# Performance work log

Hardware: AMD Instinct MI355X
Metric: run time of the kernel (lower is better)

## Reference

```python
import jax, jax.numpy as jnp
import numpy as np

N_NODES = 20000
N_EDGES = 320000
N_GRAPHS = 64
IN_FEAT = 64
HIDDEN = 256
GRID = 4
NUM_LAYERS = 4  # -> 3 Fourier message-passing layers
NEG_SLOPE = 0.01  # nn.LeakyReLU default


def setup_inputs() -> dict:
    key = jax.random.key(0)
    ks = jax.random.split(key, 8)
    h = jax.random.normal(ks[0], (N_NODES, IN_FEAT), dtype=jnp.float32)
    src = jax.random.randint(ks[1], (N_EDGES,), 0, N_NODES, dtype=jnp.int32)
    dst = jax.random.randint(ks[2], (N_EDGES,), 0, N_NODES, dtype=jnp.int32)
    graph_ids = jnp.sort(jax.random.randint(ks[3], (N_NODES,), 0, N_GRAPHS, dtype=jnp.int32))
    # KAN_polynomial(in_feat, hidden, degree=grid_feat), init randn/(sqrt(in)*sqrt(deg))
    W_line = jax.random.normal(ks[4], (HIDDEN, IN_FEAT, GRID + 1), dtype=jnp.float32) / (
        np.sqrt(IN_FEAT) * np.sqrt(GRID))
    # 3 NaiveFourierKANLayer coeffs [2, out, in, grid]
    fourier_coeffs = jax.random.normal(ks[5], (NUM_LAYERS - 1, 2, HIDDEN, HIDDEN, GRID),
                                       dtype=jnp.float32) / (np.sqrt(HIDDEN) * np.sqrt(GRID))
    # Readout KAN_polynomial(hidden, 1, degree=1, addbias=True)
    W_out = jax.random.normal(ks[6], (1, HIDDEN, 2), dtype=jnp.float32) / np.sqrt(HIDDEN)
    b_out = jnp.zeros((1, 1), dtype=jnp.float32)
    return {"h": h, "src": src, "dst": dst, "graph_ids": graph_ids,
            "W_line": W_line, "fourier_coeffs": fourier_coeffs,
            "W_out": W_out, "b_out": b_out}


def kan_polynomial(x, coeffs, bias=None):
    # x: [b, in], coeffs: [out, in, deg+1]
    deg = coeffs.shape[-1] - 1
    powers = jnp.stack([x ** i for i in range(deg + 1)], axis=-1)  # [b, in, deg+1]
    y = jnp.einsum('bid,oid->bo', powers, coeffs)
    if bias is not None:
        y = y + bias
    return y


def fourier_kan(x, coeffs):
    # x: [N, in], coeffs: [2, out, in, grid]
    grid = coeffs.shape[-1]
    k = jnp.arange(1, grid + 1, dtype=x.dtype)  # [grid]
    ang = x[:, :, None] * k  # [N, in, grid]
    y = jnp.einsum('nig,oig->no', jnp.cos(ang), coeffs[0])
    y = y + jnp.einsum('nig,oig->no', jnp.sin(ang), coeffs[1])
    return y


def reference(h, src, dst, graph_ids, W_line, fourier_coeffs, W_out, b_out):
    # kan_line
    h = kan_polynomial(h, W_line)  # [N, hidden]
    # message-passing Fourier KAN layers with residual + leaky_relu
    for l in range(NUM_LAYERS - 1):
        agg = jax.ops.segment_sum(h[src], dst, num_segments=N_NODES)  # copy_u + sum
        m = fourier_kan(agg, fourier_coeffs[l])
        h = jax.nn.leaky_relu(m + h, negative_slope=NEG_SLOPE)
    # avg pooling per graph
    sums = jax.ops.segment_sum(h, graph_ids, num_segments=N_GRAPHS)  # [G, hidden]
    counts = jax.ops.segment_sum(jnp.ones((N_NODES,), dtype=h.dtype), graph_ids,
                                 num_segments=N_GRAPHS)
    y = sums / jnp.maximum(counts, 1.0)[:, None]
    # Readout: KAN_polynomial(hidden, 1, degree=1) + sigmoid
    out = jax.nn.sigmoid(kan_polynomial(y, W_out, b_out))  # [G, 1]
    return out
```

## Files before the change

### kernel.cpp

```cpp
#include <hip/hip_runtime.h>
#include <math.h>

#define N_NODES   20000
#define N_PAD     20032
#define N_PAD2    20096
#define N_EDGES   320000
#define N_GRAPHS  64
#define IN_FEAT   64
#define HIDDEN    256
#define GRID_F    4
#define NLAYERS   3
#define NEG_SLOPE 0.01f

#define KF 2048
#define KL4 256
#define NB_SCAN 79
#define NRG  157
#define NBLK (NRG * 4)
#define NLBLK 1256

typedef _Float16 f16x8 __attribute__((ext_vector_type(8)));
typedef float    f32x4 __attribute__((ext_vector_type(4)));

__global__ void transpose_fourier_f16(const float* __restrict__ fc, _Float16* __restrict__ Bt) {
    int idx = blockIdx.x * 256 + threadIdx.x;
    int kk  = idx & 2047;
    int rest = idx >> 11;
    int o = rest & 255;
    int l = rest >> 8;
    int i = kk >> 3, f = kk & 7, t = f >> 2, g = f & 3;
    Bt[idx] = (_Float16)fc[(((size_t)(l * 2 + t) * HIDDEN + o) * HIDDEN + i) * GRID_F + g];
}

__global__ void transpose_line4(const float* __restrict__ wl, _Float16* __restrict__ Wth,
                                _Float16* __restrict__ Wtl) {
    int idx = blockIdx.x * 256 + threadIdx.x;
    int o = idx >> 8, kk = idx & 255;
    int i = kk >> 2, d = (kk & 3) + 1;
    float wv = wl[(o * IN_FEAT + i) * 5 + d];
    _Float16 h = (_Float16)wv;
    Wth[idx] = h;
    Wtl[idx] = (_Float16)(wv - (float)h);
}

__global__ void line_bias(const float* __restrict__ wl, float* __restrict__ biasv) {
    int o = threadIdx.x;
    float s = 0.f;
    for (int i = 0; i < IN_FEAT; ++i) s += wl[(o * IN_FEAT + i) * 5];
    biasv[o] = s;
}

__global__ void count_deg(const int* __restrict__ dst, int* __restrict__ counts) {
    int e = blockIdx.x * 256 + threadIdx.x;
    if (e < N_EDGES) atomicAdd(&counts[dst[e]], 1);
}

__global__ void block_sums(const int* __restrict__ counts, int* __restrict__ bsum) {
    int i = blockIdx.x * 256 + threadIdx.x;
    int v = (i < N_NODES) ? counts[i] : 0;
    #pragma unroll
    for (int o = 32; o > 0; o >>= 1) v += __shfl_down(v, o, 64);
    __shared__ int ws[4];
    if ((threadIdx.x & 63) == 0) ws[threadIdx.x >> 6] = v;
    __syncthreads();
    if (threadIdx.x == 0) bsum[blockIdx.x] = ws[0] + ws[1] + ws[2] + ws[3];
}

__global__ void scan_mid(const int* __restrict__ bsum, int* __restrict__ bofs,
                         int* __restrict__ row_start) {
    __shared__ int buf[128];
    int t = threadIdx.x;
    int v = (t < NB_SCAN) ? bsum[t] : 0;
    buf[t] = v;
    __syncthreads();
    for (int d = 1; d < 128; d <<= 1) {
        int x = (t >= d) ? buf[t - d] : 0;
        __syncthreads();
        buf[t] += x;
        __syncthreads();
    }
    if (t < NB_SCAN) bofs[t] = buf[t] - v;
    if (t == NB_SCAN - 1) row_start[N_NODES] = buf[t];
}

__global__ void scan_blocks(const int* __restrict__ counts, const int* __restrict__ bofs,
                            int* __restrict__ row_start) {
    int i = blockIdx.x * 256 + threadIdx.x;
    int val = (i < N_NODES) ? counts[i] : 0;
    int lane = threadIdx.x & 63, wid = threadIdx.x >> 6;
    int v = val;
    #pragma unroll
    for (int d = 1; d < 64; d <<= 1) {
        int t = __shfl_up(v, d, 64);
        if (lane >= d) v += t;
    }
    __shared__ int ws[4];
    if (lane == 63) ws[wid] = v;
    __syncthreads();
    int wofs = 0;
    for (int j = 0; j < wid; ++j) wofs += ws[j];
    if (i < N_NODES) row_start[i] = bofs[blockIdx.x] + wofs + v - val;
}

__global__ void fill_csr(const int* __restrict__ src, const int* __restrict__ dst,
                         const int* __restrict__ row_start, int* __restrict__ cursor,
                         int* __restrict__ ssrc) {
    int e = blockIdx.x * 256 + threadIdx.x;
    if (e < N_EDGES) {
        int d = dst[e];
        int pos = row_start[d] + atomicAdd(&cursor[d], 1);
        ssrc[pos] = src[e];
    }
}

__global__ __launch_bounds__(256)
void aggregate(const float* __restrict__ h, const int* __restrict__ row_start,
               const int* __restrict__ ssrc, float* __restrict__ agg) {
    const int node = blockIdx.x * 4 + (threadIdx.x >> 6);
    const int lane = threadIdx.x & 63;
    const int b = row_start[node], e = row_start[node + 1];
    f32x4 a0 = {0.f, 0.f, 0.f, 0.f}, a1 = {0.f, 0.f, 0.f, 0.f};
    int j = b;
    for (; j + 1 < e; j += 2) {
        int s0 = ssrc[j], s1 = ssrc[j + 1];
        a0 += *(const f32x4*)&h[(size_t)s0 * HIDDEN + lane * 4];
        a1 += *(const f32x4*)&h[(size_t)s1 * HIDDEN + lane * 4];
    }
    if (j < e) {
        int s0 = ssrc[j];
        a0 += *(const f32x4*)&h[(size_t)s0 * HIDDEN + lane * 4];
    }
    *(f32x4*)&agg[(size_t)node * HIDDEN + lane * 4] = a0 + a1;
}

__device__ __forceinline__ void makepow(float xa, float xb, f16x8& hi, f16x8& lo) {
    float p0 = xa, p1 = xa * xa;
    float p2 = p1 * xa, p3 = p1 * p1;
    float q0 = xb, q1 = xb * xb;
    float q2 = q1 * xb, q3 = q1 * q1;
    float pp[8] = {p0, p1, p2, p3, q0, q1, q2, q3};
    #pragma unroll
    for (int j = 0; j < 8; ++j) {
        _Float16 h = (_Float16)pp[j];
        hi[j] = h;
        lo[j] = (_Float16)(pp[j] - (float)h);
    }
}

__global__ __launch_bounds__(256)
void kan_line_mfma(const float* __restrict__ x, const _Float16* __restrict__ Wth,
                   const _Float16* __restrict__ Wtl, const float* __restrict__ biasv,
                   float* __restrict__ out) {
    __shared__ float    As[64][64];
    __shared__ _Float16 Bsh[64][136];
    __shared__ _Float16 Bsl[64][136];

    const int t = threadIdx.x;
    const int w = t >> 6, l = t & 63, ln = l & 15, quad = l >> 4;
    const int wr = w >> 1, wc = w & 1;

    const int g   = blockIdx.x;
    const int bid = (g & 7) * 157 + (g >> 3);
    const int Mbase = (bid >> 2) * 64;
    const int col0  = (bid & 3) * 64;

    #pragma unroll
    for (int r = 0; r < 4; ++r) {
        int idx = r * 256 + t;
        int row = idx >> 4, p = idx & 15;
        int grow = Mbase + row;
        if (grow > N_NODES - 1) grow = N_NODES - 1;
        f32x4 v = *(const f32x4*)&x[(size_t)grow * IN_FEAT + p * 4];
        *(f32x4*)&As[row][(p * 4) ^ ((row & 7) << 2)] = v;
    }
    const _Float16* WthB = Wth + (size_t)col0 * KL4;
    const _Float16* WtlB = Wtl + (size_t)col0 * KL4;
    #pragma unroll
    for (int r = 0; r < 4; ++r) {
        int idx = r * 256 + t;
        int c = idx >> 4, p = idx & 15;
        *(f16x8*)&Bsh[c][p * 8] = *(const f16x8*)&WthB[(size_t)c * KL4 + p * 8];
        *(f16x8*)&Bsl[c][p * 8] = *(const f16x8*)&WtlB[(size_t)c * KL4 + p * 8];
    }
    f16x8 pbh[4], pbl[4];
    #pragma unroll
    for (int r = 0; r < 4; ++r) {
        int idx = r * 256 + t;
        int c = idx >> 4, p = idx & 15;
        pbh[r] = *(const f16x8*)&WthB[(size_t)c * KL4 + 128 + p * 8];
        pbl[r] = *(const f16x8*)&WtlB[(size_t)c * KL4 + 128 + p * 8];
    }
    __syncthreads();

    f32x4 acc[2][2];
    #pragma unroll
    for (int rt = 0; rt < 2; ++rt)
        #pragma unroll
        for (int ct = 0; ct < 2; ++ct)
            acc[rt][ct] = (f32x4){0.f, 0.f, 0.f, 0.f};

    const int lr0 = wr * 32 + ln;
    const int xsw = (lr0 & 7) << 2;

    #pragma unroll
    for (int half = 0; half < 2; ++half) {
        #pragma unroll
        for (int kcl = 0; kcl < 4; ++kcl) {
            const int kc = half * 4 + kcl;
            const int f0 = kc * 8 + quad * 2;
            float x00 = As[lr0     ][f0 ^ xsw];
            float x01 = As[lr0     ][(f0 + 1) ^ xsw];
            float x10 = As[lr0 + 16][f0 ^ xsw];
            float x11 = As[lr0 + 16][(f0 + 1) ^ xsw];
            f16x8 ah0, al0, ah1, al1;
            makepow(x00, x01, ah0, al0);
            makepow(x10, x11, ah1, al1);
            #pragma unroll
            for (int ct = 0; ct < 2; ++ct) {
                const int bc = wc * 32 + ct * 16 + ln;
                f16x8 bh = *(const f16x8*)&Bsh[bc][kcl * 32 + quad * 8];
                f16x8 bl = *(const f16x8*)&Bsl[bc][kcl * 32 + quad * 8];
                acc[0][ct] = __builtin_amdgcn_mfma_f32_16x16x32_f16(ah0, bh, acc[0][ct], 0, 0, 0);
                acc[0][ct] = __builtin_amdgcn_mfma_f32_16x16x32_f16(al0, bh, acc[0][ct], 0, 0, 0);
                acc[0][ct] = __builtin_amdgcn_mfma_f32_16x16x32_f16(ah0, bl, acc[0][ct], 0, 0, 0);
                acc[1][ct] = __builtin_amdgcn_mfma_f32_16x16x32_f16(ah1, bh, acc[1][ct], 0, 0, 0);
                acc[1][ct] = __builtin_amdgcn_mfma_f32_16x16x32_f16(al1, bh, acc[1][ct], 0, 0, 0);
                acc[1][ct] = __builtin_amdgcn_mfma_f32_16x16x32_f16(ah1, bl, acc[1][ct], 0, 0, 0);
            }
        }
        if (half == 0) {
            __syncthreads();
            #pragma unroll
            for (int r = 0; r < 4; ++r) {
                int idx = r * 256 + t;
                int c = idx >> 4, p = idx & 15;
                *(f16x8*)&Bsh[c][p * 8] = pbh[r];
                *(f16x8*)&Bsl[c][p * 8] = pbl[r];
            }
            __syncthreads();
        }
    }

    #pragma unroll
    for (int rt = 0; rt < 2; ++rt) {
        const int row0 = Mbase + wr * 32 + rt * 16 + quad * 4;
        #pragma unroll
        for (int ct = 0; ct < 2; ++ct) {
            const int col = col0 + wc * 32 + ct * 16 + ln;
            const float bv = biasv[col];
            #pragma unroll
            for (int r = 0; r < 4; ++r) {
                const int row = row0 + r;
                if (row < N_NODES)
                    out[(size_t)row * HIDDEN + col] = acc[rt][ct][r] + bv;
            }
        }
    }
}

__device__ __forceinline__ f16x8 trig8(float xv) {
    float r = xv * 0.15915494309189535f;
    r -= floorf(r);
    float s1 = __builtin_amdgcn_sinf(r);
    float c1 = __builtin_amdgcn_cosf(r);
    float c2 = c1 * c1 - s1 * s1, s2 = 2.f * s1 * c1;
    float c3 = c2 * c1 - s2 * s1, s3 = s2 * c1 + c2 * s1;
    float c4 = c2 * c2 - s2 * s2, s4 = 2.f * s2 * c2;
    f16x8 a;
    a[0] = (_Float16)c1; a[1] = (_Float16)c2;
    a[2] = (_Float16)c3; a[3] = (_Float16)c4;
    a[4] = (_Float16)s1; a[5] = (_Float16)s2;
    a[6] = (_Float16)s3; a[7] = (_Float16)s4;
    return a;
}

__global__ __launch_bounds__(256)
void fourier_mfma(const float* __restrict__ agg, float* hio,
                  const _Float16* __restrict__ Bt) {
    __shared__ _Float16 Bs[2][64][136];
    __shared__ float    As[2][128][16];

    const int t    = threadIdx.x;
    const int w    = t >> 6;
    const int l    = t & 63;
    const int ln   = l & 15;
    const int quad = l >> 4;

    const int g   = blockIdx.x;
    const int xcd = g & 7, ii = g >> 3;
    const int bid = (xcd < 4 ? xcd * 79 : 316 + (xcd - 4) * 78) + ii;
    const int Mbase = (bid >> 2) * 128;
    const int col0  = (bid & 3) * 64;

    const int sc = t >> 4, sp = t & 15;
    const int sr = t >> 2, sq = t & 3;
    const _Float16* bg0 = Bt + (size_t)(col0 + sc) * KF + sp * 8;
    const _Float16* bg1 = bg0 + (size_t)16 * KF;
    const _Float16* bg2 = bg0 + (size_t)32 * KF;
    const _Float16* bg3 = bg0 + (size_t)48 * KF;
    const float* ag0 = agg + (size_t)(Mbase + sr) * HIDDEN + sq * 4;
    const float* ag1 = ag0 + (size_t)64 * HIDDEN;
    const int swA = (sq ^ (sr & 3)) << 2;

    f32x4 acc[2][4];
    #pragma unroll
    for (int rt = 0; rt < 2; ++rt)
        #pragma unroll
        for (int ct = 0; ct < 4; ++ct)
            acc[rt][ct] = (f32x4){0.f, 0.f, 0.f, 0.f};

    f16x8 sb0, sb1, sb2, sb3;
    f32x4 sa0, sa1;

    sb0 = *(const f16x8*)(bg0);
    sb1 = *(const f16x8*)(bg1);
    sb2 = *(const f16x8*)(bg2);
    sb3 = *(const f16x8*)(bg3);
    sa0 = *(const f32x4*)(ag0);
    sa1 = *(const f32x4*)(ag1);
    *(f16x8*)&Bs[0][sc     ][sp * 8] = sb0;
    *(f16x8*)&Bs[0][sc + 16][sp * 8] = sb1;
    *(f16x8*)&Bs[0][sc + 32][sp * 8] = sb2;
    *(f16x8*)&Bs[0][sc + 48][sp * 8] = sb3;
    *(f32x4*)&As[0][sr     ][swA] = sa0;
    *(f32x4*)&As[0][sr + 64][swA] = sa1;
    __syncthreads();

    const int lr0 = w * 32 + ln;
    const int xm  = ln & 3;

    for (int kg = 0; kg < 16; ++kg) {
        const int b = kg & 1;
        if (kg < 15) {
            sb0 = *(const f16x8*)(bg0 + (kg + 1) * 128);
            sb1 = *(const f16x8*)(bg1 + (kg + 1) * 128);
            sb2 = *(const f16x8*)(bg2 + (kg + 1) * 128);
            sb3 = *(const f16x8*)(bg3 + (kg + 1) * 128);
            sa0 = *(const f32x4*)(ag0 + (kg + 1) * 16);
            sa1 = *(const f32x4*)(ag1 + (kg + 1) * 16);
        }
        #pragma unroll
        for (int kc = 0; kc < 4; ++kc) {
            float xv0 = As[b][lr0     ][((kc ^ xm) << 2) | quad];
            float xv1 = As[b][lr0 + 16][((kc ^ xm) << 2) | quad];
            f16x8 b0 = *(const f16x8*)&Bs[b][ln     ][kc * 32 + quad * 8];
            f16x8 b1 = *(const f16x8*)&Bs[b][ln + 16][kc * 32 + quad * 8];
            f16x8 b2 = *(const f16x8*)&Bs[b][ln + 32][kc * 32 + quad * 8];
            f16x8 b3 = *(const f16x8*)&Bs[b][ln + 48][kc * 32 + quad * 8];
            f16x8 a0 = trig8(xv0);
            f16x8 a1 = trig8(xv1);
            acc[0][0] = __builtin_amdgcn_mfma_f32_16x16x32_f16(a0, b0, acc[0][0], 0, 0, 0);
            acc[0][1] = __builtin_amdgcn_mfma_f32_16x16x32_f16(a0, b1, acc[0][1], 0, 0, 0);
            acc[0][2] = __builtin_amdgcn_mfma_f32_16x16x32_f16(a0, b2, acc[0][2], 0, 0, 0);
            acc[0][3] = __builtin_amdgcn_mfma_f32_16x16x32_f16(a0, b3, acc[0][3], 0, 0, 0);
            acc[1][0] = __builtin_amdgcn_mfma_f32_16x16x32_f16(a1, b0, acc[1][0], 0, 0, 0);
            acc[1][1] = __builtin_amdgcn_mfma_f32_16x16x32_f16(a1, b1, acc[1][1], 0, 0, 0);
            acc[1][2] = __builtin_amdgcn_mfma_f32_16x16x32_f16(a1, b2, acc[1][2], 0, 0, 0);
            acc[1][3] = __builtin_amdgcn_mfma_f32_16x16x32_f16(a1, b3, acc[1][3], 0, 0, 0);
        }
        __syncthreads();
        if (kg < 15) {
            const int nb = b ^ 1;
            *(f16x8*)&Bs[nb][sc     ][sp * 8] = sb0;
            *(f16x8*)&Bs[nb][sc + 16][sp * 8] = sb1;
            *(f16x8*)&Bs[nb][sc + 32][sp * 8] = sb2;
            *(f16x8*)&Bs[nb][sc + 48][sp * 8] = sb3;
            *(f32x4*)&As[nb][sr     ][swA] = sa0;
            *(f32x4*)&As[nb][sr + 64][swA] = sa1;
        }
        __syncthreads();
    }

    #pragma unroll
    for (int rt = 0; rt < 2; ++rt) {
        const int row0 = Mbase + w * 32 + rt * 16 + quad * 4;
        #pragma unroll
        for (int ct = 0; ct < 4; ++ct) {
            const int col = col0 + ct * 16 + ln;
            #pragma unroll
            for (int r = 0; r < 4; ++r) {
                const int row = row0 + r;
                if (row < N_NODES) {
                    float v = acc[rt][ct][r] + hio[(size_t)row * HIDDEN + col];
                    v = v > 0.f ? v : NEG_SLOPE * v;
                    hio[(size_t)row * HIDDEN + col] = v;
                }
            }
        }
    }
}

__global__ void graph_bounds(const int* __restrict__ gid, int* __restrict__ gstart) {
    int g = threadIdx.x;
    if (g < N_GRAPHS) {
        int lo = 0, hi = N_NODES;
        while (lo < hi) { int mid = (lo + hi) >> 1; if (gid[mid] < g) lo = mid + 1; else hi = mid; }
        gstart[g] = lo;
    } else if (g == N_GRAPHS) {
        gstart[g] = N_NODES;
    }
}

__global__ __launch_bounds__(256)
void pool_seg(const float* __restrict__ h, const int* __restrict__ gid,
              float* __restrict__ pooled) {
    const int c = threadIdx.x;
    const int s = blockIdx.x * 128;
    const int e = min(s + 128, N_NODES);
    float acc = 0.f;
    int g = gid[s];
    for (int n = s; n < e; ++n) {
        int gn = gid[n];
        if (gn != g) {
            atomicAdd(&pooled[g * HIDDEN + c], acc);
            acc = 0.f;
            g = gn;
        }
        acc += h[(size_t)n * HIDDEN + c];
    }
    atomicAdd(&pooled[g * HIDDEN + c], acc);
}

__global__ void readout(const float* __restrict__ pooled, const int* __restrict__ gstart,
                        const float* __restrict__ wout, const float* __restrict__ bout,
                        float* __restrict__ out) {
    int g = blockIdx.x, t = threadIdx.x;
    float cnt = fmaxf((float)(gstart[g + 1] - gstart[g]), 1.f);
    float y = pooled[g * HIDDEN + t] / cnt;
    float term = wout[t * 2 + 0] + wout[t * 2 + 1] * y;
    #pragma unroll
    for (int o = 32; o > 0; o >>= 1) term += __shfl_down(term, o, 64);
    __shared__ float wsum[4];
    if ((t & 63) == 0) wsum[t >> 6] = term;
    __syncthreads();
    if (t == 0) {
        float s = wsum[0] + wsum[1] + wsum[2] + wsum[3] + bout[0];
        out[g] = 1.f / (1.f + expf(-s));
    }
}

extern "C" void kernel_launch(void* const* d_in, const int* in_sizes, int n_in,
                              void* d_out, int out_size, void* d_ws, size_t ws_size,
                              hipStream_t stream) {
    const float* h_in  = (const float*)d_in[0];
    const int*   src   = (const int*)d_in[1];
    const int*   dst   = (const int*)d_in[2];
    const int*   gid   = (const int*)d_in[3];
    const float* wline = (const float*)d_in[4];
    const float* fcoef = (const float*)d_in[5];
    const float* wout  = (const float*)d_in[6];
    const float* bout  = (const float*)d_in[7];
    float* out = (float*)d_out;

    char* ws = (char*)d_ws;
    size_t off = 0;
    auto alloc = [&](size_t bytes) {
        size_t o = off;
        off += (bytes + 255) & ~size_t(255);
        return o;
    };
    float*     hbuf      = (float*)(ws + alloc((size_t)N_PAD2 * HIDDEN * 4));
    float*     aggbuf    = (float*)(ws + alloc((size_t)N_PAD2 * HIDDEN * 4));
    _Float16*  BtF16     = (_Float16*)(ws + alloc((size_t)NLAYERS * KF * HIDDEN * 2));
    _Float16*  Wth       = (_Float16*)(ws + alloc((size_t)HIDDEN * KL4 * 2));
    _Float16*  Wtl       = (_Float16*)(ws + alloc((size_t)HIDDEN * KL4 * 2));
    float*     biasv     = (float*)(ws + alloc((size_t)HIDDEN * 4));
    int*       row_start = (int*)(ws + alloc((size_t)(N_NODES + 1) * 4));
    int*       counts    = (int*)(ws + alloc((size_t)N_NODES * 4));
    int*       cursor    = (int*)(ws + alloc((size_t)N_NODES * 4));
    int*       ssrc      = (int*)(ws + alloc((size_t)N_EDGES * 4));
    int*       bsum      = (int*)(ws + alloc((size_t)128 * 4));
    int*       bofs      = (int*)(ws + alloc((size_t)128 * 4));
    int*       gstart    = (int*)(ws + alloc((size_t)(N_GRAPHS + 1) * 4));
    float*     pooled    = (float*)(ws + alloc((size_t)N_GRAPHS * HIDDEN * 4));

    hipMemsetAsync(counts, 0, (size_t)N_NODES * 4, stream);
    hipMemsetAsync(cursor, 0, (size_t)N_NODES * 4, stream);
    hipMemsetAsync(pooled, 0, (size_t)N_GRAPHS * HIDDEN * 4, stream);
    hipMemsetAsync(aggbuf + (size_t)N_NODES * HIDDEN, 0,
                   (size_t)(N_PAD2 - N_NODES) * HIDDEN * 4, stream);

    transpose_fourier_f16<<<6144, 256, 0, stream>>>(fcoef, BtF16);
    transpose_line4<<<256, 256, 0, stream>>>(wline, Wth, Wtl);
    line_bias<<<1, 256, 0, stream>>>(wline, biasv);
    count_deg<<<(N_EDGES + 255) / 256, 256, 0, stream>>>(dst, counts);
    block_sums<<<NB_SCAN, 256, 0, stream>>>(counts, bsum);
    scan_mid<<<1, 128, 0, stream>>>(bsum, bofs, row_start);
    scan_blocks<<<NB_SCAN, 256, 0, stream>>>(counts, bofs, row_start);
    fill_csr<<<(N_EDGES + 255) / 256, 256, 0, stream>>>(src, dst, row_start, cursor, ssrc);
    graph_bounds<<<1, 128, 0, stream>>>(gid, gstart);

    kan_line_mfma<<<NLBLK, 256, 0, stream>>>(h_in, Wth, Wtl, biasv, hbuf);

    for (int l = 0; l < NLAYERS; ++l) {
        aggregate<<<N_NODES / 4, 256, 0, stream>>>(hbuf, row_start, ssrc, aggbuf);
        fourier_mfma<<<NBLK, 256, 0, stream>>>(aggbuf, hbuf,
                                               BtF16 + (size_t)l * KF * HIDDEN);
    }

    pool_seg<<<(N_NODES + 127) / 128, 256, 0, stream>>>(hbuf, gid, pooled);
    readout<<<N_GRAPHS, 256, 0, stream>>>(pooled, gstart, wout, bout, out);
}
```

Measured before the change: 470.2 us.

## Compute Fourier harmonics in packed fp16 with interleaved cos/sin layout

Rewrites the per-element trig expansion so that harmonics 2-4 come from packed half2 complex-multiply recurrences, with cos/sin pairs interleaved. The fourier weight transpose is reordered to match the new (g, t) interleaving. The shared-memory A tile switches from XOR swizzling to row padding, and the B tile padding changes. Together these aim to cut VALU work in the trig-feature generation and simplify the LDS addressing. The cost is fp16 precision in the recurrence and scalar LDS stores in place of vector stores.

```diff
diff --git a/kernel.cpp b/kernel.cpp
--- a/kernel.cpp
+++ b/kernel.cpp
@@ -2,7 +2,6 @@
 #include <math.h>
 
 #define N_NODES   20000
-#define N_PAD     20032
 #define N_PAD2    20096
 #define N_EDGES   320000
 #define N_GRAPHS  64
@@ -20,6 +19,7 @@
 #define NLBLK 1256
 
 typedef _Float16 f16x8 __attribute__((ext_vector_type(8)));
+typedef _Float16 f16x2 __attribute__((ext_vector_type(2)));
 typedef float    f32x4 __attribute__((ext_vector_type(4)));
 
 __global__ void transpose_fourier_f16(const float* __restrict__ fc, _Float16* __restrict__ Bt) {
@@ -28,7 +28,7 @@
     int rest = idx >> 11;
     int o = rest & 255;
     int l = rest >> 8;
-    int i = kk >> 3, f = kk & 7, t = f >> 2, g = f & 3;
+    int i = kk >> 3, f = kk & 7, g = f >> 1, t = f & 1;
     Bt[idx] = (_Float16)fc[(((size_t)(l * 2 + t) * HIDDEN + o) * HIDDEN + i) * GRID_F + g];
 }
 
@@ -258,27 +258,28 @@
     }
 }
 
-__device__ __forceinline__ f16x8 trig8(float xv) {
+__device__ __forceinline__ f16x8 trig8i(float xv) {
     float r = xv * 0.15915494309189535f;
     r -= floorf(r);
     float s1 = __builtin_amdgcn_sinf(r);
     float c1 = __builtin_amdgcn_cosf(r);
-    float c2 = c1 * c1 - s1 * s1, s2 = 2.f * s1 * c1;
-    float c3 = c2 * c1 - s2 * s1, s3 = s2 * c1 + c2 * s1;
-    float c4 = c2 * c2 - s2 * s2, s4 = 2.f * s2 * c2;
-    f16x8 a;
-    a[0] = (_Float16)c1; a[1] = (_Float16)c2;
-    a[2] = (_Float16)c3; a[3] = (_Float16)c4;
-    a[4] = (_Float16)s1; a[5] = (_Float16)s2;
-    a[6] = (_Float16)s3; a[7] = (_Float16)s4;
-    return a;
+    _Float16 c1h = (_Float16)c1, s1h = (_Float16)s1;
+    f16x2 z1 = {c1h, s1h};
+    f16x2 cc = {c1h, c1h};
+    f16x2 ms = {(_Float16)-s1h, s1h};
+    f16x2 z2 = z1 * cc + (f16x2){z1[1], z1[0]} * ms;
+    f16x2 z3 = z2 * cc + (f16x2){z2[1], z2[0]} * ms;
+    f16x2 z4 = z3 * cc + (f16x2){z3[1], z3[0]} * ms;
+    union { f16x8 v; f16x2 p[4]; } u;
+    u.p[0] = z1; u.p[1] = z2; u.p[2] = z3; u.p[3] = z4;
+    return u.v;
 }
 
 __global__ __launch_bounds__(256)
 void fourier_mfma(const float* __restrict__ agg, float* hio,
                   const _Float16* __restrict__ Bt) {
-    __shared__ _Float16 Bs[2][64][136];
-    __shared__ float    As[2][128][16];
+    __shared__ _Float16 Bs[2][64][140];
+    __shared__ float    As[2][128][17];
 
     const int t    = threadIdx.x;
     const int w    = t >> 6;
@@ -300,7 +301,6 @@
     const _Float16* bg3 = bg0 + (size_t)48 * KF;
     const float* ag0 = agg + (size_t)(Mbase + sr) * HIDDEN + sq * 4;
     const float* ag1 = ag0 + (size_t)64 * HIDDEN;
-    const int swA = (sq ^ (sr & 3)) << 2;
 
     f32x4 acc[2][4];
     #pragma unroll
@@ -322,12 +322,14 @@
     *(f16x8*)&Bs[0][sc + 16][sp * 8] = sb1;
     *(f16x8*)&Bs[0][sc + 32][sp * 8] = sb2;
     *(f16x8*)&Bs[0][sc + 48][sp * 8] = sb3;
-    *(f32x4*)&As[0][sr     ][swA] = sa0;
-    *(f32x4*)&As[0][sr + 64][swA] = sa1;
+    #pragma unroll
+    for (int j = 0; j < 4; ++j) {
+        As[0][sr     ][sq * 4 + j] = sa0[j];
+        As[0][sr + 64][sq * 4 + j] = sa1[j];
+    }
     __syncthreads();
 
     const int lr0 = w * 32 + ln;
-    const int xm  = ln & 3;
 
     for (int kg = 0; kg < 16; ++kg) {
         const int b = kg & 1;
@@ -341,14 +343,14 @@
         }
         #pragma unroll
         for (int kc = 0; kc < 4; ++kc) {
-            float xv0 = As[b][lr0     ][((kc ^ xm) << 2) | quad];
-            float xv1 = As[b][lr0 + 16][((kc ^ xm) << 2) | quad];
+            float xv0 = As[b][lr0     ][kc * 4 + quad];
+            float xv1 = As[b][lr0 + 16][kc * 4 + quad];
             f16x8 b0 = *(const f16x8*)&Bs[b][ln     ][kc * 32 + quad * 8];
             f16x8 b1 = *(const f16x8*)&Bs[b][ln + 16][kc * 32 + quad * 8];
             f16x8 b2 = *(const f16x8*)&Bs[b][ln + 32][kc * 32 + quad * 8];
             f16x8 b3 = *(const f16x8*)&Bs[b][ln + 48][kc * 32 + quad * 8];
-            f16x8 a0 = trig8(xv0);
-            f16x8 a1 = trig8(xv1);
+            f16x8 a0 = trig8i(xv0);
+            f16x8 a1 = trig8i(xv1);
             acc[0][0] = __builtin_amdgcn_mfma_f32_16x16x32_f16(a0, b0, acc[0][0], 0, 0, 0);
             acc[0][1] = __builtin_amdgcn_mfma_f32_16x16x32_f16(a0, b1, acc[0][1], 0, 0, 0);
             acc[0][2] = __builtin_amdgcn_mfma_f32_16x16x32_f16(a0, b2, acc[0][2], 0, 0, 0);
@@ -365,8 +367,11 @@
             *(f16x8*)&Bs[nb][sc + 16][sp * 8] = sb1;
             *(f16x8*)&Bs[nb][sc + 32][sp * 8] = sb2;
             *(f16x8*)&Bs[nb][sc + 48][sp * 8] = sb3;
-            *(f32x4*)&As[nb][sr     ][swA] = sa0;
-            *(f32x4*)&As[nb][sr + 64][swA] = sa1;
+            #pragma unroll
+            for (int j = 0; j < 4; ++j) {
+                As[nb][sr     ][sq * 4 + j] = sa0[j];
+                As[nb][sr + 64][sq * 4 + j] = sa1[j];
+            }
         }
         __syncthreads();
     }
```

New measurement: 455.2 us. -3.2%, faster.
